# Performance work log

Hardware: AMD Instinct MI355X
Metric: run time of the kernel (lower is better)

## Reference

```python
import jax, jax.numpy as jnp
import numpy as np

T_STEPS = 500
NHEAD = 4
L_TRANS = 2

def _pe(L, D):
    pos = np.arange(L)[:, None].astype(np.float32)
    i = np.arange(D // 2)[None, :].astype(np.float32)
    ang = pos / np.power(10000.0, 2.0 * i / D)
    pe = np.zeros((L, D), np.float32)
    pe[:, 0::2] = np.sin(ang)
    pe[:, 1::2] = np.cos(ang)
    return jnp.asarray(pe)

def _ln(x, g, b):
    m = x.mean(-1, keepdims=True)
    v = ((x - m) ** 2).mean(-1, keepdims=True)
    return (x - m) / jnp.sqrt(v + 1e-5) * g + b

def _gcn(A, X, W1, b1, W2, b2, W3, b3):
    h = jax.nn.relu((A @ X) @ W1 + b1)
    h = jax.nn.relu((A @ h) @ W2 + b2)
    return (A @ h) @ W3 + b3

def _mha(h, Wq, bq, Wk, bk, Wv, bv, Wo, bo):
    B, L, D = h.shape
    dh = D // NHEAD
    q = (h @ Wq + bq).reshape(B, L, NHEAD, dh)
    k = (h @ Wk + bk).reshape(B, L, NHEAD, dh)
    v = (h @ Wv + bv).reshape(B, L, NHEAD, dh)
    s = jnp.einsum('blhd,bmhd->bhlm', q, k) / jnp.sqrt(jnp.float32(dh))
    a = jax.nn.softmax(s, axis=-1)
    o = jnp.einsum('bhlm,bmhd->blhd', a, v).reshape(B, L, D)
    return o @ Wo + bo


def setup_inputs() -> dict:
    key = jax.random.key(0)
    ks = jax.random.split(key, 24)
    N_FP, N_WORD, DIM, HID = 10000, 4096, 20, 512
    HD1, HD2, LOUT, TDIM, FF = 128, 64, 3, 20, 2048
    N_ATOMS, N_RES, N_EDGES = 256, 4096, 65536
    w = lambda k, shp, s=0.05: jax.random.normal(k, shp, jnp.float32) * s
    idx_aa = jax.random.randint(ks[0], (N_RES,), 0, 20)
    x = jax.nn.one_hot(idx_aa, 20, dtype=jnp.float32)  # node one-hots
    adj_s = (jax.random.uniform(ks[1], (N_ATOMS, N_ATOMS)) < 0.1).astype(jnp.float32)
    return dict(
        x=x,
        smileadjacency=adj_s,
        emb_fp=w(ks[2], (N_FP, DIM)),
        emb_word=w(ks[3], (N_WORD, HID), 0.02),
        gW1=w(ks[4], (DIM, HD1)), gb1=jnp.zeros((HD1,), jnp.float32),
        gW2=w(ks[5], (HD1, HD2)), gb2=jnp.zeros((HD2,), jnp.float32),
        gW3=w(ks[6], (HD2, DIM)), gb3=jnp.zeros((DIM,), jnp.float32),
        Wq=w(ks[7], (L_TRANS, HID, HID)), bq=jnp.zeros((L_TRANS, HID), jnp.float32),
        Wk=w(ks[8], (L_TRANS, HID, HID)), bk=jnp.zeros((L_TRANS, HID), jnp.float32),
        Wv=w(ks[9], (L_TRANS, HID, HID)), bv=jnp.zeros((L_TRANS, HID), jnp.float32),
        Wo=w(ks[10], (L_TRANS, HID, HID)), bo=jnp.zeros((L_TRANS, HID), jnp.float32),
        ln1g=jnp.ones((L_TRANS, HID), jnp.float32), ln1b=jnp.zeros((L_TRANS, HID), jnp.float32),
        Wff1=w(ks[11], (L_TRANS, HID, FF)), bff1=jnp.zeros((L_TRANS, FF), jnp.float32),
        Wff2=w(ks[12], (L_TRANS, FF, HID)), bff2=jnp.zeros((L_TRANS, HID), jnp.float32),
        ln2g=jnp.ones((L_TRANS, HID), jnp.float32), ln2b=jnp.zeros((L_TRANS, HID), jnp.float32),
        Wproj=w(ks[13], (HID, DIM)), bproj=jnp.zeros((DIM,), jnp.float32),
        Wout=w(ks[14], (LOUT, 4 * DIM, 4 * DIM)), bout=jnp.zeros((LOUT, 4 * DIM), jnp.float32),
        Wtime=w(ks[15], (1, TDIM)), btime=jnp.zeros((TDIM,), jnp.float32),
        fingerprints=jax.random.randint(ks[16], (N_ATOMS,), 0, N_FP),
        words=jax.random.randint(ks[17], (N_RES,), 0, N_WORD),
        batch=jnp.zeros((N_RES,), jnp.int32),
        edge_index=jax.random.randint(ks[18], (2, N_EDGES), 0, N_RES),
        t=250,
        layer_output=3,
        dropout=0,
    )


def reference(x, smileadjacency, emb_fp, emb_word, gW1, gb1, gW2, gb2, gW3, gb3,
              Wq, bq, Wk, bk, Wv, bv, Wo, bo, ln1g, ln1b, Wff1, bff1, Wff2, bff2,
              ln2g, ln2b, Wproj, bproj, Wout, bout, Wtime, btime,
              fingerprints, words, batch, edge_index, t, layer_output, dropout):
    # --- diffusion noise (cosine alpha_bar, blosum-style transition, uniform mixing) ---
    t_float = float(t) / T_STEPS
    s = 0.008
    ab = np.cos((t_float + s) / (1 + s) * np.pi / 2) ** 2 / (np.cos(s / (1 + s) * np.pi / 2) ** 2)
    ab = jnp.float32(ab)
    Qtb = ab * jnp.eye(20, dtype=jnp.float32) + (1.0 - ab) / 20.0  # [20,20]
    prob = jnp.einsum('nij,nj->ni', Qtb[None][batch], x[:, :20])    # [n,20]
    X_t = jax.random.categorical(jax.random.key(42), jnp.log(prob + 1e-9))
    X = jax.nn.one_hot(X_t, 20, dtype=jnp.float32)
    time_emb = jnp.array([[t_float]], jnp.float32) @ Wtime + btime  # [1,20]
    # --- substrate GCN ---
    fp_vec = emb_fp[fingerprints]                                   # [n_atoms, dim]
    sub = _gcn(smileadjacency, fp_vec, gW1, gb1, gW2, gb2, gW3, gb3).mean(0, keepdims=True)
    # --- sequence transformer ---
    h = emb_word[words][None] + _pe(words.shape[0], emb_word.shape[1])[None]  # [1,L,hid]
    for l in range(L_TRANS):
        a = _mha(h, Wq[l], bq[l], Wk[l], bk[l], Wv[l], bv[l], Wo[l], bo[l])
        h = _ln(h + a, ln1g[l], ln1b[l])
        ff = jax.nn.relu(h @ Wff1[l] + bff1[l]) @ Wff2[l] + bff2[l]
        h = _ln(h + ff, ln2g[l], ln2b[l])
    seq = (h[0] @ Wproj + bproj).mean(0, keepdims=True)             # [1,dim]
    # --- protein graph: vectorized adjacency scatter (replaces per-edge python loop) ---
    n = X.shape[0]
    adj = jnp.zeros((n, n), jnp.float32).at[edge_index[0], edge_index[1]].set(1.0)
    prot = _gcn(adj, X, gW1, gb1, gW2, gb2, gW3, gb3).mean(0, keepdims=True)
    # --- fusion head (dropout=0 / eval mode) ---
    cat = jnp.concatenate([sub, prot, seq, time_emb], axis=1)        # [1, 4*dim]
    for j in range(int(layer_output)):
        cat = jax.nn.relu(cat) @ Wout[j] + bout[j]
    cat = jax.nn.relu(cat)
    return (cat, seq)
```

## Files before the change

kernel.cpp:

```cpp
#include <hip/hip_runtime.h>
#include <math.h>

typedef unsigned short ushort_t;
typedef __attribute__((ext_vector_type(8))) short bf16x8;
typedef __attribute__((ext_vector_type(4))) float f32x4;

__device__ inline float bf2f(unsigned u) { return __uint_as_float((u & 0xffffu) << 16); }
__device__ inline ushort_t f2bf(float f) {
    unsigned u = __float_as_uint(f);
    return (ushort_t)((u + 0x7fffu + ((u >> 16) & 1u)) >> 16);
}
__device__ inline void stv(float* p, float v) { *p = v; }
__device__ inline void stv(ushort_t* p, float v) { *p = f2bf(v); }
__device__ inline int guard_int(int raw, int lo, int hi) {
    if (raw >= lo && raw <= hi) return raw;
    float f = __int_as_float(raw);
    int v = (int)f;
    return (v >= lo && v <= hi) ? v : lo;
}

__device__ inline void tf2x32(unsigned k0, unsigned k1, unsigned x0, unsigned x1,
                              unsigned& o0, unsigned& o1) {
    unsigned ks2 = k0 ^ k1 ^ 0x1BD11BDAu;
    x0 += k0; x1 += k1;
#define TFR(r) { x0 += x1; x1 = (x1 << (r)) | (x1 >> (32 - (r))); x1 ^= x0; }
    TFR(13) TFR(15) TFR(26) TFR(6)  x0 += k1;  x1 += ks2 + 1u;
    TFR(17) TFR(29) TFR(16) TFR(24) x0 += ks2; x1 += k0 + 2u;
    TFR(13) TFR(15) TFR(26) TFR(6)  x0 += k0;  x1 += k1 + 3u;
    TFR(17) TFR(29) TFR(16) TFR(24) x0 += k1;  x1 += ks2 + 4u;
    TFR(13) TFR(15) TFR(26) TFR(6)  x0 += ks2; x1 += k0 + 5u;
#undef TFR
    o0 = x0; o1 = x1;
}

__global__ void k_sentinel(float* __restrict__ out, float val, int n) {
    int i = blockIdx.x * 128 + threadIdx.x;
    if (i < n) out[i] = val;
}

__global__ __launch_bounds__(256) void k_sample(const float* __restrict__ x,
                                                const int* __restrict__ t_ptr,
                                                float* __restrict__ X) {
    int i = blockIdx.x * 256 + threadIdx.x;
    if (i >= 4096) return;
    int tval = guard_int(t_ptr[0], 0, 500);
    double tf = (double)tval / 500.0;
    const double sc = 0.008;
    const double PI_HALF = 1.5707963267948966;
    double num = cos((tf + sc) / (1.0 + sc) * PI_HALF);
    double den = cos(sc / (1.0 + sc) * PI_HALF);
    float ab = (float)((num * num) / (den * den));
    float phi = (1.0f - ab) / 20.0f;
    float xv[20]; float sx = 0.f;
    for (int j = 0; j < 20; ++j) { xv[j] = x[i * 20 + j]; sx += xv[j]; }
    float best = -1e30f; int bj = 0;
    for (int j = 0; j < 20; ++j) {
        float prob = fmaxf(ab * xv[j] + phi * sx, 0.0f);
        float lp = logf(prob + 1e-9f);
        unsigned m = (unsigned)(i * 20 + j);
        unsigned o0, o1;
        tf2x32(0u, 42u, 0u, m, o0, o1);
        unsigned bits = o0 ^ o1;
        float u = __uint_as_float((bits >> 9) | 0x3f800000u) - 1.0f;
        if (u < 1.1754943508222875e-38f) u = 1.1754943508222875e-38f;
        float gmb = -logf(-logf(u));
        float z = lp + gmb;
        if (z > best) { best = z; bj = j; }
    }
    for (int j = 0; j < 20; ++j) X[i * 20 + j] = (j == bj) ? 1.0f : 0.0f;
}

__global__ __launch_bounds__(256) void k_gather_fp(const float* __restrict__ emb,
                                                   const int* __restrict__ idx,
                                                   float* __restrict__ out) {
    int i = blockIdx.x * 256 + threadIdx.x;
    if (i >= 256 * 20) return;
    int a = i / 20, d = i % 20;
    out[i] = emb[(size_t)idx[a] * 20 + d];
}

__global__ __launch_bounds__(256) void k_scatter_bits(const int* __restrict__ ei,
                                                      unsigned* __restrict__ bits) {
    int e = blockIdx.x * 256 + threadIdx.x;
    if (e >= 65536) return;
    int r = ei[e], c = ei[65536 + e];
    atomicOr(&bits[(size_t)r * 128 + (c >> 5)], 1u << (c & 31));
}

__global__ __launch_bounds__(256) void k_degree(const unsigned* __restrict__ BITS,
                                                float* __restrict__ deg) {
    int i = blockIdx.x * 256 + threadIdx.x;
    if (i >= 4096 * 128) return;
    unsigned bits = BITS[i];
    int base = (i & 127) * 32;
    while (bits) { int b = __ffs(bits) - 1; bits &= bits - 1; atomicAdd(&deg[base + b], 1.0f); }
}

__global__ __launch_bounds__(256) void k_embed(const float* __restrict__ embw,
                                               const int* __restrict__ words,
                                               float* __restrict__ H,
                                               ushort_t* __restrict__ Hb) {
    int idx = blockIdx.x * 256 + threadIdx.x;
    if (idx >= 4096 * 512) return;
    int pos = idx >> 9, d = idx & 511;
    float e = embw[(size_t)words[pos] * 512 + d];
    float expo = (float)(d >> 1) * (1.0f / 256.0f);
    float ang = (float)pos * exp2f(-expo * 13.287712379549449f);
    float pe = (d & 1) ? cosf(ang) : sinf(ang);
    float v = e + pe;
    H[idx] = v; Hb[idx] = f2bf(v);
}

__global__ __launch_bounds__(256) void k_colmean(const float* __restrict__ M, int R, int C,
                                                 float* __restrict__ out) {
    __shared__ float red[256];
    int c = blockIdx.x, t = threadIdx.x;
    float s = 0.f;
    for (int r = t; r < R; r += 256) s += M[(size_t)r * C + c];
    red[t] = s; __syncthreads();
    for (int o = 128; o; o >>= 1) { if (t < o) red[t] += red[t + o]; __syncthreads(); }
    if (t == 0) out[c] = red[0] / (float)R;
}

__global__ __launch_bounds__(256) void k_wcolsum(const float* __restrict__ M, int R, int C,
                                                 const float* __restrict__ w,
                                                 float* __restrict__ out) {
    __shared__ float red[256];
    int c = blockIdx.x, t = threadIdx.x;
    float s = 0.f;
    for (int r = t; r < R; r += 256) s += w[r] * M[(size_t)r * C + c];
    red[t] = s; __syncthreads();
    for (int o = 128; o; o >>= 1) { if (t < o) red[t] += red[t + o]; __syncthreads(); }
    if (t == 0) out[c] = red[0];
}

__global__ __launch_bounds__(256) void k_matvec20(int D, float scale,
                                                  const float* __restrict__ vec,
                                                  const float* __restrict__ W,
                                                  const float* __restrict__ bias,
                                                  float* __restrict__ out) {
    __shared__ float red[256];
    int c = blockIdx.x, t = threadIdx.x;
    float s = 0.f;
    for (int d = t; d < D; d += 256) s += vec[d] * W[(size_t)d * 20 + c];
    red[t] = s; __syncthreads();
    for (int o = 128; o; o >>= 1) { if (t < o) red[t] += red[t + o]; __syncthreads(); }
    if (t == 0) out[c] = red[0] * scale + bias[c];
}

__global__ __launch_bounds__(256) void k_castT(const float* __restrict__ in,
                                               ushort_t* __restrict__ out,
                                               int Kd, int Nd) {
    __shared__ float t[32][33];
    int bx = blockIdx.x * 32, by = blockIdx.y * 32;
    int tx = threadIdx.x & 31, ty = threadIdx.x >> 5;
#pragma unroll
    for (int i = 0; i < 4; ++i)
        t[ty + i * 8][tx] = in[(size_t)(by + ty + i * 8) * Nd + bx + tx];
    __syncthreads();
#pragma unroll
    for (int i = 0; i < 4; ++i)
        out[(size_t)(bx + ty + i * 8) * Kd + by + tx] = f2bf(t[tx][ty + i * 8]);
}

__global__ __launch_bounds__(256) void k_transposeV(const ushort_t* __restrict__ in, int ldin,
                                                    ushort_t* __restrict__ out) {
    __shared__ ushort_t t[32][33];
    int bx = blockIdx.x * 32;
    int by = blockIdx.y * 32;
    int tx = threadIdx.x & 31, ty = threadIdx.x >> 5;
#pragma unroll
    for (int i = 0; i < 4; ++i)
        t[ty + i * 8][tx] = in[(size_t)(by + ty + i * 8) * ldin + bx + tx];
    __syncthreads();
#pragma unroll
    for (int i = 0; i < 4; ++i)
        out[(size_t)(bx + ty + i * 8) * 4096 + by + tx] = t[tx][ty + i * 8];
}

template<int BN, bool RELU, typename TC>
__global__ __launch_bounds__(256) void k_gemm_mfma2(int M, int N, int K, int lda,
        const ushort_t* __restrict__ A,
        const ushort_t* __restrict__ Bt,
        TC* __restrict__ C, int ldc,
        const float* __restrict__ bias) {
    constexpr int NJ = BN / 32;
    __shared__ ushort_t As[128][40];
    __shared__ ushort_t Bs[BN][40];
    int tid = threadIdx.x;
    int lane = tid & 63, wave = tid >> 6;
    int wr = wave >> 1, wc = wave & 1;
    int lrow = lane & 15, lq = lane >> 4;
    int br = blockIdx.y * 128, bc = blockIdx.x * BN;
    f32x4 acc[4][NJ];
#pragma unroll
    for (int i = 0; i < 4; ++i)
#pragma unroll
        for (int j = 0; j < NJ; ++j) { acc[i][j][0] = 0.f; acc[i][j][1] = 0.f; acc[i][j][2] = 0.f; acc[i][j][3] = 0.f; }
    int sr = tid >> 2, sseg = tid & 3;
    for (int k0 = 0; k0 < K; k0 += 32) {
#pragma unroll
        for (int it = 0; it < 2; ++it)
            *(uint4*)&As[sr + it * 64][sseg * 8] = *(const uint4*)&A[(size_t)(br + sr + it * 64) * lda + k0 + sseg * 8];
#pragma unroll
        for (int it = 0; it < BN / 64; ++it)
            *(uint4*)&Bs[sr + it * 64][sseg * 8] = *(const uint4*)&Bt[(size_t)(bc + sr + it * 64) * K + k0 + sseg * 8];
        __syncthreads();
        bf16x8 af[4], bfr[NJ];
#pragma unroll
        for (int i = 0; i < 4; ++i) af[i] = *(const bf16x8*)&As[wr * 64 + i * 16 + lrow][lq * 8];
#pragma unroll
        for (int j = 0; j < NJ; ++j) bfr[j] = *(const bf16x8*)&Bs[wc * (BN / 2) + j * 16 + lrow][lq * 8];
#pragma unroll
        for (int i = 0; i < 4; ++i)
#pragma unroll
            for (int j = 0; j < NJ; ++j)
                acc[i][j] = __builtin_amdgcn_mfma_f32_16x16x32_bf16(af[i], bfr[j], acc[i][j], 0, 0, 0);
        __syncthreads();
    }
#pragma unroll
    for (int i = 0; i < 4; ++i)
#pragma unroll
        for (int j = 0; j < NJ; ++j) {
            int col = bc + wc * (BN / 2) + j * 16 + lrow;
            float bv = bias ? bias[col] : 0.f;
#pragma unroll
            for (int r = 0; r < 4; ++r) {
                int row = br + wr * 64 + i * 16 + lq * 4 + r;
                float v = acc[i][j][r] + bv;
                if (RELU) v = fmaxf(v, 0.f);
                stv(&C[(size_t)row * ldc + col], v);
            }
        }
}

template<bool RELU>
__global__ __launch_bounds__(256) void k_gemm_nn(int M, int N, int K,
        const float* __restrict__ A, int lda,
        const float* __restrict__ B, int ldb,
        float* __restrict__ C, int ldc,
        const float* __restrict__ bias) {
    __shared__ float As[16][65];
    __shared__ float Bs[16][65];
    int tid = threadIdx.x;
    int tx = tid & 15, ty = tid >> 4;
    int br = blockIdx.y * 64, bc = blockIdx.x * 64;
    float acc[4][4] = {};
    for (int k0 = 0; k0 < K; k0 += 16) {
#pragma unroll
        for (int c0 = 0; c0 < 4; ++c0) {
            int r = (tid >> 4) + c0 * 16, kk = tid & 15;
            int gr = br + r, gk = k0 + kk;
            As[kk][r] = (gr < M && gk < K) ? A[(size_t)gr * lda + gk] : 0.f;
        }
#pragma unroll
        for (int c0 = 0; c0 < 4; ++c0) {
            int col = tid & 63, kk = (tid >> 6) + c0 * 4;
            int gc = bc + col, gk = k0 + kk;
            Bs[kk][col] = (gc < N && gk < K) ? B[(size_t)gk * ldb + gc] : 0.f;
        }
        __syncthreads();
#pragma unroll
        for (int kk = 0; kk < 16; ++kk) {
            float av[4], bv[4];
#pragma unroll
            for (int i2 = 0; i2 < 4; ++i2) av[i2] = As[kk][ty + 16 * i2];
#pragma unroll
            for (int j2 = 0; j2 < 4; ++j2) bv[j2] = Bs[kk][tx + 16 * j2];
#pragma unroll
            for (int i2 = 0; i2 < 4; ++i2)
#pragma unroll
                for (int j2 = 0; j2 < 4; ++j2) acc[i2][j2] += av[i2] * bv[j2];
        }
        __syncthreads();
    }
#pragma unroll
    for (int i2 = 0; i2 < 4; ++i2)
#pragma unroll
        for (int j2 = 0; j2 < 4; ++j2) {
            int r = br + ty + 16 * i2, c = bc + tx + 16 * j2;
            if (r < M && c < N) {
                float v = acc[i2][j2];
                if (bias) v += bias[c];
                if (RELU) v = fmaxf(v, 0.f);
                C[(size_t)r * ldc + c] = v;
            }
        }
}

template<int NC, int CH>
__global__ __launch_bounds__(256) void k_spmm_wave(
        const unsigned* __restrict__ BITS,
        const float* __restrict__ B, int ldb,
        float* __restrict__ C, int ldc) {
    int gw = blockIdx.x * 4 + (threadIdx.x >> 6);
    int lane = threadIdx.x & 63;
    int row = gw / CH, cb = (gw % CH) * NC;
    if (row >= 4096) return;
    float acc[NC];
#pragma unroll
    for (int j = 0; j < NC; ++j) acc[j] = 0.f;
    const unsigned* bw = &BITS[(size_t)row * 128];
#pragma unroll
    for (int i = 0; i < 2; ++i) {
        int wd = lane * 2 + i;
        unsigned bits = bw[wd];
        int base = wd * 32;
        while (bits) {
            int b = __ffs(bits) - 1; bits &= bits - 1;
            const float* br = &B[(size_t)(base + b) * ldb + cb];
#pragma unroll
            for (int j = 0; j < NC; ++j) acc[j] += br[j];
        }
    }
#pragma unroll
    for (int j = 0; j < NC; ++j) {
#pragma unroll
        for (int off = 1; off < 64; off <<= 1) acc[j] += __shfl_xor(acc[j], off, 64);
    }
    if (lane == 0)
#pragma unroll
        for (int j = 0; j < NC; ++j) C[(size_t)row * ldc + cb + j] = acc[j];
}

__global__ __launch_bounds__(256) void k_flash(const ushort_t* __restrict__ Qg, int ldq,
                                               const ushort_t* __restrict__ Kg, int ldk,
                                               const ushort_t* __restrict__ VTg,
                                               ushort_t* __restrict__ OP,
                                               float* __restrict__ Mp,
                                               float* __restrict__ Lp) {
    __shared__ ushort_t Ks[32][136];
    __shared__ ushort_t Vt[128][40];
    __shared__ ushort_t Ps[4][16][40];
    __shared__ float    as_[4][16];
    __shared__ float    ls_[4][16];
    const int tid = threadIdx.x;
    const int lane = tid & 63, wid = tid >> 6;
    const int lrow = lane & 15, lq = lane >> 4;
    const int qb = blockIdx.x * 64, hh = blockIdx.y, z = blockIdx.z;
    const float scale = 0.08838834764831845f;
    bf16x8 qf[4];
    {
        const ushort_t* qrow = &Qg[(size_t)(qb + wid * 16 + lrow) * ldq + hh * 128 + lq * 8];
#pragma unroll
        for (int s = 0; s < 4; ++s) qf[s] = *(const bf16x8*)&qrow[s * 32];
    }
    f32x4 o[8];
#pragma unroll
    for (int ct = 0; ct < 8; ++ct) { o[ct][0] = 0.f; o[ct][1] = 0.f; o[ct][2] = 0.f; o[ct][3] = 0.f; }
    float m = -INFINITY, l = 0.f;
    for (int kt = z * 64; kt < z * 64 + 64; ++kt) {
#pragma unroll
        for (int i = 0; i < 2; ++i) {
            int sid = tid + i * 256;
            int r = sid >> 4, sg = sid & 15;
            *(uint4*)&Ks[r][sg * 8] = *(const uint4*)&Kg[(size_t)(kt * 32 + r) * ldk + hh * 128 + sg * 8];
            int d = sid >> 2, c8 = sid & 3;
            *(uint4*)&Vt[d][c8 * 8] = *(const uint4*)&VTg[(size_t)(hh * 128 + d) * 4096 + kt * 32 + c8 * 8];
        }
        __syncthreads();
        f32x4 sa[2];
#pragma unroll
        for (int c = 0; c < 2; ++c) { sa[c][0] = 0.f; sa[c][1] = 0.f; sa[c][2] = 0.f; sa[c][3] = 0.f; }
#pragma unroll
        for (int c = 0; c < 2; ++c)
#pragma unroll
            for (int st = 0; st < 4; ++st) {
                bf16x8 kf = *(const bf16x8*)&Ks[c * 16 + lrow][st * 32 + lq * 8];
                sa[c] = __builtin_amdgcn_mfma_f32_16x16x32_bf16(kf, qf[st], sa[c], 0, 0, 0);
            }
        float s[8];
        float tm = -INFINITY;
#pragma unroll
        for (int c = 0; c < 2; ++c)
#pragma unroll
            for (int r = 0; r < 4; ++r) { float v = sa[c][r] * scale; s[c * 4 + r] = v; tm = fmaxf(tm, v); }
        tm = fmaxf(tm, __shfl_xor(tm, 16));
        tm = fmaxf(tm, __shfl_xor(tm, 32));
        float mn = fmaxf(m, tm);
        float a = expf(m - mn);
        float su = 0.f;
        float p[8];
#pragma unroll
        for (int i = 0; i < 8; ++i) { p[i] = expf(s[i] - mn); su += p[i]; }
        su += __shfl_xor(su, 16);
        su += __shfl_xor(su, 32);
        m = mn; l = l * a + su;
#pragma unroll
        for (int c = 0; c < 2; ++c)
#pragma unroll
            for (int r = 0; r < 4; ++r)
                Ps[wid][lrow][c * 16 + lq * 4 + r] = f2bf(p[c * 4 + r]);
        if (lq == 0) as_[wid][lrow] = a;
        __builtin_amdgcn_s_waitcnt(0);
        float av[4];
#pragma unroll
        for (int r = 0; r < 4; ++r) av[r] = as_[wid][lq * 4 + r];
#pragma unroll
        for (int ct = 0; ct < 8; ++ct)
#pragma unroll
            for (int r = 0; r < 4; ++r) o[ct][r] *= av[r];
        bf16x8 pf = *(const bf16x8*)&Ps[wid][lrow][lq * 8];
#pragma unroll
        for (int ct = 0; ct < 8; ++ct) {
            bf16x8 vf = *(const bf16x8*)&Vt[ct * 16 + lrow][lq * 8];
            o[ct] = __builtin_amdgcn_mfma_f32_16x16x32_bf16(pf, vf, o[ct], 0, 0, 0);
        }
        __syncthreads();
    }
    if (lq == 0) {
        Mp[(size_t)(z * 4 + hh) * 4096 + qb + wid * 16 + lrow] = m;
        Lp[(size_t)(z * 4 + hh) * 4096 + qb + wid * 16 + lrow] = l;
    }
    ushort_t* ob = OP + (size_t)z * 2097152;
#pragma unroll
    for (int ct = 0; ct < 8; ++ct)
#pragma unroll
        for (int r = 0; r < 4; ++r)
            ob[(size_t)(qb + wid * 16 + lq * 4 + r) * 512 + hh * 128 + ct * 16 + lrow] = f2bf(o[ct][r]);
}

__global__ __launch_bounds__(256) void k_fcomb(const ushort_t* __restrict__ OP,
                                               const float* __restrict__ Mp,
                                               const float* __restrict__ Lp,
                                               ushort_t* __restrict__ Ob) {
    int idx = blockIdx.x * 256 + threadIdx.x;
    if (idx >= 4096 * 512) return;
    int row = idx >> 9, col = idx & 511;
    int hh = col >> 7;
    float m0 = Mp[hh * 4096 + row], m1 = Mp[(4 + hh) * 4096 + row];
    float l0 = Lp[hh * 4096 + row], l1 = Lp[(4 + hh) * 4096 + row];
    float mm = fmaxf(m0, m1);
    float w0 = expf(m0 - mm), w1 = expf(m1 - mm);
    float denom = l0 * w0 + l1 * w1;
    float o0 = bf2f(OP[idx]), o1 = bf2f(OP[2097152 + idx]);
    Ob[idx] = f2bf((o0 * w0 + o1 * w1) / denom);
}

__global__ __launch_bounds__(256) void k_add_ln(const float* __restrict__ A,
                                                const float* __restrict__ B,
                                                float* __restrict__ O,
                                                ushort_t* __restrict__ Ob,
                                                const float* __restrict__ g,
                                                const float* __restrict__ b) {
    __shared__ float xr[512];
    __shared__ float red[256];
    int row = blockIdx.x, t = threadIdx.x;
    const float* a = A + (size_t)row * 512;
    const float* bb = B + (size_t)row * 512;
    float ls = 0.f;
    for (int j = t; j < 512; j += 256) { float v = a[j] + bb[j]; xr[j] = v; ls += v; }
    red[t] = ls; __syncthreads();
    for (int o = 128; o; o >>= 1) { if (t < o) red[t] += red[t + o]; __syncthreads(); }
    float mean = red[0] / 512.0f; __syncthreads();
    float lv = 0.f;
    for (int j = t; j < 512; j += 256) { float d = xr[j] - mean; lv += d * d; }
    red[t] = lv; __syncthreads();
    for (int o = 128; o; o >>= 1) { if (t < o) red[t] += red[t + o]; __syncthreads(); }
    float inv = 1.0f / sqrtf(red[0] / 512.0f + 1e-5f);
    float* o_ = O + (size_t)row * 512;
    ushort_t* ob = Ob + (size_t)row * 512;
    for (int j = t; j < 512; j += 256) {
        float v = (xr[j] - mean) * inv * g[j] + b[j];
        o_[j] = v; ob[j] = f2bf(v);
    }
}

__global__ __launch_bounds__(128) void k_fusion(const float* __restrict__ subv,
                                                const float* __restrict__ protv,
                                                const float* __restrict__ seqv,
                                                const float* __restrict__ Wtime,
                                                const float* __restrict__ btime,
                                                const float* __restrict__ Wout,
                                                const float* __restrict__ bout,
                                                const int* __restrict__ t_ptr,
                                                const int* __restrict__ lo_ptr,
                                                float* __restrict__ out) {
    __shared__ float cat[80];
    int t = threadIdx.x;
    int tval = guard_int(t_ptr[0], 0, 500);
    int L    = guard_int(lo_ptr[0], 0, 3);
    float tf = (float)((double)tval / 500.0);
    if (t < 20) {
        cat[t] = subv[t];
        cat[20 + t] = protv[t];
        cat[40 + t] = seqv[t];
        cat[60 + t] = tf * Wtime[t] + btime[t];
    }
    __syncthreads();
    for (int j = 0; j < L; ++j) {
        float acc = 0.f;
        if (t < 80) {
            for (int i2 = 0; i2 < 80; ++i2)
                acc += fmaxf(cat[i2], 0.f) * Wout[(size_t)j * 6400 + i2 * 80 + t];
            acc += bout[j * 80 + t];
        }
        __syncthreads();
        if (t < 80) cat[t] = acc;
        __syncthreads();
    }
    if (t < 80) out[t] = fmaxf(cat[t], 0.f);
    if (t < 20) out[80 + t] = seqv[t];
}

extern "C" void kernel_launch(void* const* d_in, const int* in_sizes, int n_in,
                              void* d_out, int out_size, void* d_ws, size_t ws_size,
                              hipStream_t stream) {
    static const int EXP[39] = {
        81920, 65536, 200000, 2097152, 2560, 128, 8192, 64, 1280, 20,
        524288, 1024, 524288, 1024, 524288, 1024, 524288, 1024, 1024, 1024,
        2097152, 4096, 2097152, 1024, 1024, 1024, 10240, 20, 19200, 240,
        20, 20, 256, 4096, 4096, 131072, 1, 1, 1 };
    float code = 0.f;
    if (n_in != 39) code = 900.f;
    else {
        for (int i = 0; i < 39; ++i)
            if (in_sizes[i] != EXP[i]) { code = 500.f + 4.f * (float)i; break; }
    }
    const size_t REQ = (size_t)46 * 1024 * 1024;
    if (code == 0.f && ws_size < REQ) code = (float)(ws_size >> 20);
    float* out = (float*)d_out;
    if (code != 0.f) {
        k_sentinel<<<1, 128, 0, stream>>>(out, -code, out_size);
        return;
    }

    const float* x_in   = (const float*)d_in[0];
    const float* adjs_in= (const float*)d_in[1];
    const float* embfp  = (const float*)d_in[2];
    const float* embw   = (const float*)d_in[3];
    const float* gW1 = (const float*)d_in[4];  const float* gb1 = (const float*)d_in[5];
    const float* gW2 = (const float*)d_in[6];  const float* gb2 = (const float*)d_in[7];
    const float* gW3 = (const float*)d_in[8];  const float* gb3 = (const float*)d_in[9];
    const float* Wq  = (const float*)d_in[10]; const float* bq  = (const float*)d_in[11];
    const float* Wk  = (const float*)d_in[12]; const float* bk  = (const float*)d_in[13];
    const float* Wv  = (const float*)d_in[14]; const float* bv  = (const float*)d_in[15];
    const float* Wo  = (const float*)d_in[16]; const float* bo  = (const float*)d_in[17];
    const float* ln1g= (const float*)d_in[18]; const float* ln1b= (const float*)d_in[19];
    const float* Wff1= (const float*)d_in[20]; const float* bff1= (const float*)d_in[21];
    const float* Wff2= (const float*)d_in[22]; const float* bff2= (const float*)d_in[23];
    const float* ln2g= (const float*)d_in[24]; const float* ln2b= (const float*)d_in[25];
    const float* Wproj=(const float*)d_in[26]; const float* bproj=(const float*)d_in[27];
    const float* Woutw=(const float*)d_in[28]; const float* boutw=(const float*)d_in[29];
    const float* Wtime=(const float*)d_in[30]; const float* btime=(const float*)d_in[31];
    const int* fingerprints = (const int*)d_in[32];
    const int* words        = (const int*)d_in[33];
    const int* edge_index   = (const int*)d_in[35];
    const int* t_ptr        = (const int*)d_in[36];
    const int* lo_ptr       = (const int*)d_in[37];

    char* wsb = (char*)d_ws;
    float*    misc = (float*)wsb;
    float*    H    = (float*)(wsb + ((size_t)2  << 20));
    ushort_t* Hb   = (ushort_t*)(wsb + ((size_t)10 << 20));
    ushort_t* QKVb = (ushort_t*)(wsb + ((size_t)14 << 20));
    ushort_t* Ob   = (ushort_t*)(wsb + ((size_t)26 << 20));
    ushort_t* FFHb = (ushort_t*)(wsb + ((size_t)14 << 20));
    float*    T    = (float*)(wsb + ((size_t)30 << 20));
    ushort_t* OP   = (ushort_t*)(wsb + ((size_t)30 << 20));
    ushort_t* Wscr = (ushort_t*)(wsb + ((size_t)38 << 20));
    ushort_t* VTg  = (ushort_t*)(wsb + ((size_t)42 << 20));
    unsigned* ADJB = (unsigned*)(wsb + ((size_t)26 << 20));
    float* pt0  = (float*)(wsb + ((size_t)14 << 20));
    float* ph1  = pt0 + 81920;
    float* pt1  = ph1 + 524288;
    float* ph2  = pt1 + 524288;
    float* Xoh  = misc;
    float* fpv  = misc + 81920;
    float* st0  = misc + 87040;
    float* sh1  = misc + 92160;
    float* st1  = misc + 124928;
    float* sh2  = misc + 157696;
    float* st2  = misc + 174080;
    float* sgo  = misc + 190464;
    float* subv = misc + 277504;
    float* protv= misc + 277536;
    float* seqv = misc + 277568;
    float* hmean= misc + 280000;
    float* wsum = misc + 281000;
    float* deg  = misc + 282000;
    float* bqkv = misc + 287000;
    float* Mp   = misc + 300000;
    float* Lp   = misc + 360000;

    auto g2 = [](int M, int N) { return dim3((unsigned)((N + 63) / 64), (unsigned)((M + 63) / 64), 1); };
    auto gm64  = [](int M, int N) { return dim3((unsigned)(N / 64), (unsigned)(M / 128), 1); };
    auto gm128 = [](int M, int N) { return dim3((unsigned)(N / 128), (unsigned)(M / 128), 1); };
    auto gt = [](int Kd, int Nd) { return dim3((unsigned)(Nd / 32), (unsigned)(Kd / 32), 1); };

    k_sample<<<16, 256, 0, stream>>>(x_in, t_ptr, Xoh);

    k_gather_fp<<<20, 256, 0, stream>>>(embfp, fingerprints, fpv);
    k_gemm_nn<false><<<g2(256, 20), 256, 0, stream>>>(256, 20, 256, adjs_in, 256, fpv, 20, st0, 20, nullptr);
    k_gemm_nn<true ><<<g2(256, 128), 256, 0, stream>>>(256, 128, 20, st0, 20, gW1, 128, sh1, 128, gb1);
    k_gemm_nn<false><<<g2(256, 128), 256, 0, stream>>>(256, 128, 256, adjs_in, 256, sh1, 128, st1, 128, nullptr);
    k_gemm_nn<true ><<<g2(256, 64), 256, 0, stream>>>(256, 64, 128, st1, 128, gW2, 64, sh2, 64, gb2);
    k_gemm_nn<false><<<g2(256, 64), 256, 0, stream>>>(256, 64, 256, adjs_in, 256, sh2, 64, st2, 64, nullptr);
    k_gemm_nn<false><<<g2(256, 20), 256, 0, stream>>>(256, 20, 64, st2, 64, gW3, 20, sgo, 20, gb3);
    k_colmean<<<20, 256, 0, stream>>>(sgo, 256, 20, subv);

    k_embed<<<8192, 256, 0, stream>>>(embw, words, H, Hb);
    for (int l = 0; l < 2; ++l) {
        k_castT<<<gt(512, 512), 256, 0, stream>>>(Wq + (size_t)l * 262144, Wscr, 512, 512);
        k_castT<<<gt(512, 512), 256, 0, stream>>>(Wk + (size_t)l * 262144, Wscr + 262144, 512, 512);
        k_castT<<<gt(512, 512), 256, 0, stream>>>(Wv + (size_t)l * 262144, Wscr + 524288, 512, 512);
        k_castT<<<gt(512, 512), 256, 0, stream>>>(Wo + (size_t)l * 262144, Wscr + 786432, 512, 512);
        hipMemcpyAsync(bqkv,        bq + l * 512, 2048, hipMemcpyDeviceToDevice, stream);
        hipMemcpyAsync(bqkv + 512,  bk + l * 512, 2048, hipMemcpyDeviceToDevice, stream);
        hipMemcpyAsync(bqkv + 1024, bv + l * 512, 2048, hipMemcpyDeviceToDevice, stream);
        k_gemm_mfma2<64, false, ushort_t><<<gm64(4096, 1536), 256, 0, stream>>>(4096, 1536, 512, 512, Hb, Wscr, QKVb, 1536, bqkv);
        k_transposeV<<<dim3(16, 128, 1), 256, 0, stream>>>(QKVb + 1024, 1536, VTg);
        k_flash<<<dim3(64, 4, 2), 256, 0, stream>>>(QKVb, 1536, QKVb + 512, 1536, VTg, OP, Mp, Lp);
        k_fcomb<<<8192, 256, 0, stream>>>(OP, Mp, Lp, Ob);
        k_gemm_mfma2<64, false, float><<<gm64(4096, 512), 256, 0, stream>>>(4096, 512, 512, 512, Ob, Wscr + 786432, T, 512, bo + l * 512);
        k_add_ln<<<4096, 256, 0, stream>>>(H, T, H, Hb, ln1g + l * 512, ln1b + l * 512);
        k_castT<<<gt(512, 2048), 256, 0, stream>>>(Wff1 + (size_t)l * 1048576, Wscr, 512, 2048);
        k_gemm_mfma2<128, true, ushort_t><<<gm128(4096, 2048), 256, 0, stream>>>(4096, 2048, 512, 512, Hb, Wscr, FFHb, 2048, bff1 + l * 2048);
        k_castT<<<gt(2048, 512), 256, 0, stream>>>(Wff2 + (size_t)l * 1048576, Wscr, 2048, 512);
        k_gemm_mfma2<64, false, float><<<gm64(4096, 512), 256, 0, stream>>>(4096, 512, 2048, 2048, FFHb, Wscr, T, 512, bff2 + l * 512);
        k_add_ln<<<4096, 256, 0, stream>>>(H, T, H, Hb, ln2g + l * 512, ln2b + l * 512);
    }

    k_colmean<<<512, 256, 0, stream>>>(H, 4096, 512, hmean);
    k_matvec20<<<20, 256, 0, stream>>>(512, 1.0f, hmean, Wproj, bproj, seqv);

    hipMemsetAsync(ADJB, 0, (size_t)4096 * 128 * 4, stream);
    hipMemsetAsync(deg, 0, 4096 * 4, stream);
    k_scatter_bits<<<256, 256, 0, stream>>>(edge_index, ADJB);
    k_spmm_wave<20, 1><<<1024, 256, 0, stream>>>(ADJB, Xoh, 20, pt0, 20);
    k_gemm_nn<true ><<<g2(4096, 128), 256, 0, stream>>>(4096, 128, 20, pt0, 20, gW1, 128, ph1, 128, gb1);
    k_spmm_wave<32, 4><<<4096, 256, 0, stream>>>(ADJB, ph1, 128, pt1, 128);
    k_gemm_nn<true ><<<g2(4096, 64), 256, 0, stream>>>(4096, 64, 128, pt1, 128, gW2, 64, ph2, 64, gb2);
    k_degree<<<2048, 256, 0, stream>>>(ADJB, deg);
    k_wcolsum<<<64, 256, 0, stream>>>(ph2, 4096, 64, deg, wsum);
    k_matvec20<<<20, 256, 0, stream>>>(64, 1.0f / 4096.0f, wsum, gW3, gb3, protv);

    k_fusion<<<1, 128, 0, stream>>>(subv, protv, seqv, Wtime, btime, Woutw, boutw, t_ptr, lo_ptr, out);
}
```

Baseline: 948.9 us.

## Split flash attention keys three ways, skip rescale, batch weight casts

Flash attention now splits the 128 key tiles across three z-slices instead of two, growing the grid from 512 to 768 blocks so more compute units are busy. The combine kernel merges three partials and writes the result in place into slice 0. Softmax now uses fast __expf and skips rescaling the output accumulator when no row maximum rose in the wave. Separately, the four QKV/O weight cast launches are merged into one, and three bias memcpys become a single gather kernel. The trade-offs are more partial traffic and combine work, an uneven 43/43/42 split, and slightly less accurate exponentials.

After: 870.0 us. 1.09x faster.

```diff
diff --git a/kernel.cpp b/kernel.cpp
--- a/kernel.cpp
+++ b/kernel.cpp
@@ -148,6 +148,13 @@
     if (t == 0) out[c] = red[0] * scale + bias[c];
 }
 
+__global__ void k_gather3(const float* __restrict__ a, const float* __restrict__ b,
+                          const float* __restrict__ c, float* __restrict__ out) {
+    int i = blockIdx.x * 256 + threadIdx.x;
+    if (i >= 1536) return;
+    out[i] = (i < 512) ? a[i] : (i < 1024) ? b[i - 512] : c[i - 1024];
+}
+
 __global__ __launch_bounds__(256) void k_castT(const float* __restrict__ in,
                                                ushort_t* __restrict__ out,
                                                int Kd, int Nd) {
@@ -161,6 +168,26 @@
 #pragma unroll
     for (int i = 0; i < 4; ++i)
         out[(size_t)(bx + ty + i * 8) * Kd + by + tx] = f2bf(t[tx][ty + i * 8]);
+}
+
+__global__ __launch_bounds__(256) void k_castT4(const float* __restrict__ in0,
+                                                const float* __restrict__ in1,
+                                                const float* __restrict__ in2,
+                                                const float* __restrict__ in3,
+                                                ushort_t* __restrict__ out) {
+    __shared__ float t[32][33];
+    int z = blockIdx.z;
+    const float* in = (z == 0) ? in0 : (z == 1) ? in1 : (z == 2) ? in2 : in3;
+    ushort_t* o = out + (size_t)z * 262144;
+    int bx = blockIdx.x * 32, by = blockIdx.y * 32;
+    int tx = threadIdx.x & 31, ty = threadIdx.x >> 5;
+#pragma unroll
+    for (int i = 0; i < 4; ++i)
+        t[ty + i * 8][tx] = in[(size_t)(by + ty + i * 8) * 512 + bx + tx];
+    __syncthreads();
+#pragma unroll
+    for (int i = 0; i < 4; ++i)
+        o[(size_t)(bx + ty + i * 8) * 512 + by + tx] = f2bf(t[tx][ty + i * 8]);
 }
 
 __global__ __launch_bounds__(256) void k_transposeV(const ushort_t* __restrict__ in, int ldin,
@@ -326,7 +353,8 @@
 __global__ __launch_bounds__(256) void k_flash(const ushort_t* __restrict__ Qg, int ldq,
                                                const ushort_t* __restrict__ Kg, int ldk,
                                                const ushort_t* __restrict__ VTg,
-                                               ushort_t* __restrict__ OP,
+                                               ushort_t* __restrict__ OP0,
+                                               ushort_t* __restrict__ OP12,
                                                float* __restrict__ Mp,
                                                float* __restrict__ Lp) {
     __shared__ ushort_t Ks[32][136];
@@ -338,6 +366,7 @@
     const int lane = tid & 63, wid = tid >> 6;
     const int lrow = lane & 15, lq = lane >> 4;
     const int qb = blockIdx.x * 64, hh = blockIdx.y, z = blockIdx.z;
+    const int kt0 = z * 43, kt1 = (z == 2) ? 128 : kt0 + 43;
     const float scale = 0.08838834764831845f;
     bf16x8 qf[4];
     {
@@ -349,7 +378,7 @@
 #pragma unroll
     for (int ct = 0; ct < 8; ++ct) { o[ct][0] = 0.f; o[ct][1] = 0.f; o[ct][2] = 0.f; o[ct][3] = 0.f; }
     float m = -INFINITY, l = 0.f;
-    for (int kt = z * 64; kt < z * 64 + 64; ++kt) {
+    for (int kt = kt0; kt < kt1; ++kt) {
 #pragma unroll
         for (int i = 0; i < 2; ++i) {
             int sid = tid + i * 256;
@@ -377,12 +406,13 @@
             for (int r = 0; r < 4; ++r) { float v = sa[c][r] * scale; s[c * 4 + r] = v; tm = fmaxf(tm, v); }
         tm = fmaxf(tm, __shfl_xor(tm, 16));
         tm = fmaxf(tm, __shfl_xor(tm, 32));
-        float mn = fmaxf(m, tm);
-        float a = expf(m - mn);
+        bool up = tm > m;
+        float mn = up ? tm : m;
+        float a = up ? __expf(m - mn) : 1.0f;
         float su = 0.f;
         float p[8];
 #pragma unroll
-        for (int i = 0; i < 8; ++i) { p[i] = expf(s[i] - mn); su += p[i]; }
+        for (int i = 0; i < 8; ++i) { p[i] = __expf(s[i] - mn); su += p[i]; }
         su += __shfl_xor(su, 16);
         su += __shfl_xor(su, 32);
         m = mn; l = l * a + su;
@@ -391,15 +421,19 @@
 #pragma unroll
             for (int r = 0; r < 4; ++r)
                 Ps[wid][lrow][c * 16 + lq * 4 + r] = f2bf(p[c * 4 + r]);
-        if (lq == 0) as_[wid][lrow] = a;
-        __builtin_amdgcn_s_waitcnt(0);
-        float av[4];
-#pragma unroll
-        for (int r = 0; r < 4; ++r) av[r] = as_[wid][lq * 4 + r];
-#pragma unroll
-        for (int ct = 0; ct < 8; ++ct)
-#pragma unroll
-            for (int r = 0; r < 4; ++r) o[ct][r] *= av[r];
+        if (__any(up)) {
+            if (lq == 0) as_[wid][lrow] = a;
+            __builtin_amdgcn_s_waitcnt(0);
+            float av[4];
+#pragma unroll
+            for (int r = 0; r < 4; ++r) av[r] = as_[wid][lq * 4 + r];
+#pragma unroll
+            for (int ct = 0; ct < 8; ++ct)
+#pragma unroll
+                for (int r = 0; r < 4; ++r) o[ct][r] *= av[r];
+        } else {
+            __builtin_amdgcn_s_waitcnt(0);
+        }
         bf16x8 pf = *(const bf16x8*)&Ps[wid][lrow][lq * 8];
 #pragma unroll
         for (int ct = 0; ct < 8; ++ct) {
@@ -412,7 +446,7 @@
         Mp[(size_t)(z * 4 + hh) * 4096 + qb + wid * 16 + lrow] = m;
         Lp[(size_t)(z * 4 + hh) * 4096 + qb + wid * 16 + lrow] = l;
     }
-    ushort_t* ob = OP + (size_t)z * 2097152;
+    ushort_t* ob = (z == 0) ? OP0 : OP12 + (size_t)(z - 1) * 2097152;
 #pragma unroll
     for (int ct = 0; ct < 8; ++ct)
 #pragma unroll
@@ -420,21 +454,21 @@
             ob[(size_t)(qb + wid * 16 + lq * 4 + r) * 512 + hh * 128 + ct * 16 + lrow] = f2bf(o[ct][r]);
 }
 
-__global__ __launch_bounds__(256) void k_fcomb(const ushort_t* __restrict__ OP,
+__global__ __launch_bounds__(256) void k_fcomb(ushort_t* __restrict__ OP0,
+                                               const ushort_t* __restrict__ OP12,
                                                const float* __restrict__ Mp,
-                                               const float* __restrict__ Lp,
-                                               ushort_t* __restrict__ Ob) {
+                                               const float* __restrict__ Lp) {
     int idx = blockIdx.x * 256 + threadIdx.x;
     if (idx >= 4096 * 512) return;
     int row = idx >> 9, col = idx & 511;
     int hh = col >> 7;
-    float m0 = Mp[hh * 4096 + row], m1 = Mp[(4 + hh) * 4096 + row];
-    float l0 = Lp[hh * 4096 + row], l1 = Lp[(4 + hh) * 4096 + row];
-    float mm = fmaxf(m0, m1);
-    float w0 = expf(m0 - mm), w1 = expf(m1 - mm);
-    float denom = l0 * w0 + l1 * w1;
-    float o0 = bf2f(OP[idx]), o1 = bf2f(OP[2097152 + idx]);
-    Ob[idx] = f2bf((o0 * w0 + o1 * w1) / denom);
+    float m0 = Mp[hh * 4096 + row], m1 = Mp[(4 + hh) * 4096 + row], m2 = Mp[(8 + hh) * 4096 + row];
+    float l0 = Lp[hh * 4096 + row], l1 = Lp[(4 + hh) * 4096 + row], l2 = Lp[(8 + hh) * 4096 + row];
+    float mm = fmaxf(m0, fmaxf(m1, m2));
+    float w0 = __expf(m0 - mm), w1 = __expf(m1 - mm), w2 = __expf(m2 - mm);
+    float denom = l0 * w0 + l1 * w1 + l2 * w2;
+    float o0 = bf2f(OP0[idx]), o1 = bf2f(OP12[idx]), o2 = bf2f(OP12[2097152 + idx]);
+    OP0[idx] = f2bf((o0 * w0 + o1 * w1 + o2 * w2) / denom);
 }
 
 __global__ __launch_bounds__(256) void k_add_ln(const float* __restrict__ A,
@@ -557,7 +591,7 @@
     ushort_t* Ob   = (ushort_t*)(wsb + ((size_t)26 << 20));
     ushort_t* FFHb = (ushort_t*)(wsb + ((size_t)14 << 20));
     float*    T    = (float*)(wsb + ((size_t)30 << 20));
-    ushort_t* OP   = (ushort_t*)(wsb + ((size_t)30 << 20));
+    ushort_t* OP12 = (ushort_t*)(wsb + ((size_t)30 << 20));
     ushort_t* Wscr = (ushort_t*)(wsb + ((size_t)38 << 20));
     ushort_t* VTg  = (ushort_t*)(wsb + ((size_t)42 << 20));
     unsigned* ADJB = (unsigned*)(wsb + ((size_t)26 << 20));
@@ -601,17 +635,13 @@
 
     k_embed<<<8192, 256, 0, stream>>>(embw, words, H, Hb);
     for (int l = 0; l < 2; ++l) {
-        k_castT<<<gt(512, 512), 256, 0, stream>>>(Wq + (size_t)l * 262144, Wscr, 512, 512);
-        k_castT<<<gt(512, 512), 256, 0, stream>>>(Wk + (size_t)l * 262144, Wscr + 262144, 512, 512);
-        k_castT<<<gt(512, 512), 256, 0, stream>>>(Wv + (size_t)l * 262144, Wscr + 524288, 512, 512);
-        k_castT<<<gt(512, 512), 256, 0, stream>>>(Wo + (size_t)l * 262144, Wscr + 786432, 512, 512);
-        hipMemcpyAsync(bqkv,        bq + l * 512, 2048, hipMemcpyDeviceToDevice, stream);
-        hipMemcpyAsync(bqkv + 512,  bk + l * 512, 2048, hipMemcpyDeviceToDevice, stream);
-        hipMemcpyAsync(bqkv + 1024, bv + l * 512, 2048, hipMemcpyDeviceToDevice, stream);
+        k_castT4<<<dim3(16, 16, 4), 256, 0, stream>>>(Wq + (size_t)l * 262144, Wk + (size_t)l * 262144,
+                                                      Wv + (size_t)l * 262144, Wo + (size_t)l * 262144, Wscr);
+        k_gather3<<<6, 256, 0, stream>>>(bq + l * 512, bk + l * 512, bv + l * 512, bqkv);
         k_gemm_mfma2<64, false, ushort_t><<<gm64(4096, 1536), 256, 0, stream>>>(4096, 1536, 512, 512, Hb, Wscr, QKVb, 1536, bqkv);
         k_transposeV<<<dim3(16, 128, 1), 256, 0, stream>>>(QKVb + 1024, 1536, VTg);
-        k_flash<<<dim3(64, 4, 2), 256, 0, stream>>>(QKVb, 1536, QKVb + 512, 1536, VTg, OP, Mp, Lp);
-        k_fcomb<<<8192, 256, 0, stream>>>(OP, Mp, Lp, Ob);
+        k_flash<<<dim3(64, 4, 3), 256, 0, stream>>>(QKVb, 1536, QKVb + 512, 1536, VTg, Ob, OP12, Mp, Lp);
+        k_fcomb<<<8192, 256, 0, stream>>>(Ob, OP12, Mp, Lp);
         k_gemm_mfma2<64, false, float><<<gm64(4096, 512), 256, 0, stream>>>(4096, 512, 512, 512, Ob, Wscr + 786432, T, 512, bo + l * 512);
         k_add_ln<<<4096, 256, 0, stream>>>(H, T, H, Hb, ln1g + l * 512, ln1b + l * 512);
         k_castT<<<gt(512, 2048), 256, 0, stream>>>(Wff1 + (size_t)l * 1048576, Wscr, 512, 2048);
```
